# Kernel optimization log

Hardware: AMD Instinct MI355X
Metric: run time of the kernel (lower is better)

## Reference

```python
import jax, jax.numpy as jnp
import numpy as np

H = 2048          # hidden_size
NH = 32           # num_attention_heads
NKV = 8           # num_key_value_heads
HD = H // NH      # head_dim = 64
ROT = int(HD * 0.25)  # rotary_ndims = 16
THETA = 10000.0


def _rope_cos_sin(seq_len, position_ids):
    # inv_freq over the rotary dims
    inv_freq = 1.0 / (THETA ** (jnp.arange(0, ROT, 2, dtype=jnp.float32) / ROT))
    t = jnp.arange(seq_len, dtype=jnp.float32)
    freqs = jnp.outer(t, inv_freq)              # [S, ROT/2]
    emb = jnp.concatenate([freqs, freqs], -1)   # [S, ROT]
    cos = jnp.cos(emb)[position_ids][:, None]   # [B, 1, Q, ROT]
    sin = jnp.sin(emb)[position_ids][:, None]
    return cos, sin


def _rotate_half(x):
    x1, x2 = jnp.split(x, 2, axis=-1)
    return jnp.concatenate([-x2, x1], axis=-1)


def setup_inputs() -> dict:
    key = jax.random.key(0)
    ks = jax.random.split(key, 5)
    B, S = 2, 2048
    hidden_states = jax.random.normal(ks[0], (B, S, H), jnp.float32)
    # additive causal mask
    neg = jnp.finfo(jnp.float32).min
    causal = jnp.where(jnp.tril(jnp.ones((S, S), bool)), 0.0, neg).astype(jnp.float32)
    attention_mask = jnp.broadcast_to(causal[None, None], (B, 1, S, S))
    position_ids = jnp.broadcast_to(jnp.arange(S, dtype=jnp.int32)[None], (B, S))
    sc = 0.02
    Wq = jax.random.normal(ks[1], (H, H), jnp.float32) * sc
    Wk = jax.random.normal(ks[2], (NKV * HD, H), jnp.float32) * sc
    Wv = jax.random.normal(ks[3], (NKV * HD, H), jnp.float32) * sc
    Wo = jax.random.normal(ks[4], (H, H), jnp.float32) * sc
    return {"hidden_states": hidden_states, "attention_mask": attention_mask,
            "position_ids": position_ids, "Wq": Wq, "Wk": Wk, "Wv": Wv, "Wo": Wo}


def reference(hidden_states, attention_mask, position_ids, Wq, Wk, Wv, Wo):
    B, S, _ = hidden_states.shape
    q = (hidden_states @ Wq.T).reshape(B, S, NH, HD).transpose(0, 2, 1, 3)    # [B,NH,S,HD]
    k = (hidden_states @ Wk.T).reshape(B, S, NKV, HD).transpose(0, 2, 1, 3)   # [B,NKV,S,HD]
    v = (hidden_states @ Wv.T).reshape(B, S, NKV, HD).transpose(0, 2, 1, 3)

    cos, sin = _rope_cos_sin(S, position_ids)  # [B,1,S,ROT]
    q_rot, q_pass = q[..., :ROT], q[..., ROT:]
    k_rot, k_pass = k[..., :ROT], k[..., ROT:]
    q_rot = q_rot * cos + _rotate_half(q_rot) * sin
    k_rot = k_rot * cos + _rotate_half(k_rot) * sin
    q = jnp.concatenate([q_rot, q_pass], -1)
    k = jnp.concatenate([k_rot, k_pass], -1)

    # GQA without materializing repeated K/V: group Q heads per KV head
    G = NH // NKV
    qg = q.reshape(B, NKV, G, S, HD)
    scores = jnp.einsum('bhgqd,bhkd->bhgqk', qg, k) / np.sqrt(HD)
    scores = scores.reshape(B, NH, S, S) + attention_mask
    probs = jax.nn.softmax(scores.astype(jnp.float32), axis=-1).astype(q.dtype)
    out = jnp.einsum('bhgqk,bhkd->bhgqd', probs.reshape(B, NKV, G, S, S), v)
    out = out.reshape(B, NH, S, HD).transpose(0, 2, 1, 3).reshape(B, S, H)
    return out @ Wo.T
```

## Files before the change

kernel.cpp:

```cpp
#include <hip/hip_runtime.h>

typedef unsigned short u16;
typedef short s16x8 __attribute__((ext_vector_type(8)));
typedef u16 u16x8 __attribute__((ext_vector_type(8)));
typedef float f32x4 __attribute__((ext_vector_type(4)));
typedef __bf16 bf16x8 __attribute__((ext_vector_type(8)));

#define B_ 2
#define S_ 2048
#define H_ 2048
#define NH_ 32
#define NKV_ 8
#define HD_ 64
#define LDQ_ 3072
#define NTOK (B_ * S_)

__device__ __forceinline__ u16 f2bf(float f) {
  unsigned u = __float_as_uint(f);
  u += 0x7fffu + ((u >> 16) & 1u);
  return (u16)(u >> 16);
}
__device__ __forceinline__ float bf2f(u16 h) {
  return __uint_as_float(((unsigned)h) << 16);
}

__device__ __forceinline__ void gload16(const void* g, void* l) {
  __builtin_amdgcn_global_load_lds(
      (const __attribute__((address_space(1))) unsigned int*)g,
      (__attribute__((address_space(3))) unsigned int*)l, 16, 0, 0);
}

__device__ __forceinline__ f32x4 mfma16(s16x8 a, s16x8 b, f32x4 c) {
  return __builtin_amdgcn_mfma_f32_16x16x32_bf16(
      __builtin_bit_cast(bf16x8, a), __builtin_bit_cast(bf16x8, b), c, 0, 0, 0);
}

__global__ __launch_bounds__(256) void cvt_bf16(const float* __restrict__ src,
                                                u16* __restrict__ dst, int n8) {
  int i = blockIdx.x * 256 + threadIdx.x;
  if (i >= n8) return;
  const float4* s = (const float4*)src + (size_t)i * 2;
  float4 a = s[0], b = s[1];
  u16x8 o;
  o[0] = f2bf(a.x); o[1] = f2bf(a.y); o[2] = f2bf(a.z); o[3] = f2bf(a.w);
  o[4] = f2bf(b.x); o[5] = f2bf(b.y); o[6] = f2bf(b.z); o[7] = f2bf(b.w);
  *((u16x8*)dst + i) = o;
}

__global__ __launch_bounds__(256) void rope_table(float* __restrict__ tab) {
  int i = blockIdx.x * 256 + threadIdx.x;
  if (i >= S_ * 8) return;
  int p = i >> 3, k = i & 7;
  float inv = powf(10000.0f, -(float)k * 0.125f);
  float ang = (float)p * inv;
  tab[p * 16 + k] = cosf(ang);
  tab[p * 16 + 8 + k] = sinf(ang);
}

__global__ __launch_bounds__(256) void rope_apply(u16* __restrict__ C,
                                                  const int* __restrict__ pos,
                                                  const float* __restrict__ tab) {
  int t = blockIdx.x * 256 + threadIdx.x;
  if (t >= NTOK * 40) return;
  int token = t / 40, hh = t - token * 40;
  u16* p = C + (size_t)token * LDQ_ + (hh < 32 ? hh * 64 : 2048 + (hh - 32) * 64);
  const float* ct = tab + (size_t)pos[token] * 16;
  float x[16];
#pragma unroll
  for (int i = 0; i < 16; ++i) x[i] = bf2f(p[i]);
#pragma unroll
  for (int i = 0; i < 8; ++i) {
    float c = ct[i], s = ct[8 + i];
    p[i]     = f2bf(x[i] * c - x[i + 8] * s);
    p[i + 8] = f2bf(x[i + 8] * c + x[i] * s);
  }
}

__global__ __launch_bounds__(256) void vtrans(const u16* __restrict__ C,
                                              u16* __restrict__ Vt) {
  __shared__ u16 tile[64][72];
  int st = blockIdx.x;
  int kv = blockIdx.y;
  int tid = threadIdx.x;
  const u16* src = C + ((size_t)(kv >> 3) * S_ + (size_t)st * 64) * LDQ_ + 2560 + (kv & 7) * 64;
#pragma unroll
  for (int it = 0; it < 2; ++it) {
    int c = it * 256 + tid;
    int s = c >> 3, d0 = (c & 7) * 8;
    *(u16x8*)&tile[s][d0] = *(const u16x8*)(src + (size_t)s * LDQ_ + d0);
  }
  __syncthreads();
  u16* dst = Vt + (size_t)kv * HD_ * S_ + st * 64;
  int s = tid & 63;
#pragma unroll
  for (int it = 0; it < 16; ++it) {
    int d = it * 4 + (tid >> 6);
    dst[(size_t)d * S_ + s] = tile[s][d];
  }
}

__device__ __forceinline__ void store_c(u16* p, float v) { *p = f2bf(v); }
__device__ __forceinline__ void store_c(float* p, float v) { *p = v; }

template <typename OutT>
__global__ __launch_bounds__(256, 3) void gemm_bt(const u16* __restrict__ A,
                                                  const u16* __restrict__ Bw,
                                                  OutT* __restrict__ C,
                                                  int M, int N, int K) {
  __shared__ u16 lds[2 * 128 * 64];
  u16* ldsA = lds;
  u16* ldsB = lds + 128 * 64;
  const int tid = threadIdx.x;
  const int lane = tid & 63;
  const int wave = tid >> 6;
  const int wm = (wave & 1) * 64;
  const int wn = (wave >> 1) * 64;
  const int m0 = blockIdx.y * 128;
  const int n0 = blockIdx.x * 128;
  const int l15 = lane & 15;
  const int quad = lane >> 4;

  f32x4 acc[4][4];
#pragma unroll
  for (int i = 0; i < 4; ++i)
#pragma unroll
    for (int j = 0; j < 4; ++j) acc[i][j] = {0.f, 0.f, 0.f, 0.f};

  const u16* Ab = A + (size_t)m0 * K;
  const u16* Bb = Bw + (size_t)n0 * K;

  for (int k0 = 0; k0 < K; k0 += 64) {
    __syncthreads();
#pragma unroll
    for (int it = 0; it < 4; ++it) {
      int c = it * 256 + tid;
      int row = c >> 3;
      int kk = (c & 7) * 8;
      gload16(Ab + (size_t)row * K + k0 + kk, ldsA + (size_t)c * 8);
      gload16(Bb + (size_t)row * K + k0 + kk, ldsB + (size_t)c * 8);
    }
    __syncthreads();
#pragma unroll
    for (int ks = 0; ks < 2; ++ks) {
      int ko = ks * 32 + quad * 8;
      s16x8 af[4], bfr[4];
#pragma unroll
      for (int i = 0; i < 4; ++i)
        af[i] = *(const s16x8*)(ldsA + (size_t)(wm + i * 16 + l15) * 64 + ko);
#pragma unroll
      for (int j = 0; j < 4; ++j)
        bfr[j] = *(const s16x8*)(ldsB + (size_t)(wn + j * 16 + l15) * 64 + ko);
#pragma unroll
      for (int i = 0; i < 4; ++i)
#pragma unroll
        for (int j = 0; j < 4; ++j)
          acc[i][j] = mfma16(af[i], bfr[j], acc[i][j]);
    }
  }
#pragma unroll
  for (int i = 0; i < 4; ++i) {
    int row = m0 + wm + i * 16 + quad * 4;
#pragma unroll
    for (int j = 0; j < 4; ++j) {
      int col = n0 + wn + j * 16 + l15;
#pragma unroll
      for (int r = 0; r < 4; ++r) store_c(C + (size_t)(row + r) * N + col, acc[i][j][r]);
    }
  }
}

#define KSTRIDE 72
#define PSTRIDE 72
__global__ __launch_bounds__(256, 3) void flash_attn(const u16* __restrict__ QKV,
                                                     const u16* __restrict__ Vt,
                                                     u16* __restrict__ O) {
  __shared__ u16 Kl2[2][64 * KSTRIDE];
  __shared__ u16 Vl2[2][64 * KSTRIDE];
  __shared__ u16 Pb[4][16 * PSTRIDE];
  const int h = blockIdx.x;
  const int b = blockIdx.y;
  const int qt = 15 - (int)blockIdx.z;
  const int kvh = h >> 2;
  const int tid = threadIdx.x;
  const int lane = tid & 63;
  const int wave = tid >> 6;
  const int l15 = lane & 15;
  const int quad = lane >> 4;

  const u16* Qb = QKV + (size_t)b * S_ * LDQ_ + h * 64;
  const u16* Kb = QKV + (size_t)b * S_ * LDQ_ + 2048 + kvh * 64;
  const u16* Vb = Vt + (size_t)(b * 8 + kvh) * HD_ * S_;

  s16x8 qf[2][2];
#pragma unroll
  for (int g = 0; g < 2; ++g) {
    int qrow = qt * 128 + wave * 32 + g * 16 + l15;
#pragma unroll
    for (int ks = 0; ks < 2; ++ks)
      qf[g][ks] = *(const s16x8*)(Qb + (size_t)qrow * LDQ_ + ks * 32 + quad * 8);
  }

  f32x4 acc_o[2][4];
#pragma unroll
  for (int g = 0; g < 2; ++g)
#pragma unroll
    for (int nt = 0; nt < 4; ++nt) acc_o[g][nt] = {0.f, 0.f, 0.f, 0.f};
  float l_lane[2][4];
#pragma unroll
  for (int g = 0; g < 2; ++g)
#pragma unroll
    for (int r = 0; r < 4; ++r) l_lane[g][r] = 0.0f;

  const int r0 = tid >> 3, ch0 = (tid & 7) * 8;
  const int r1 = (tid + 256) >> 3, ch1 = (tid & 7) * 8;

  const int nkt = 2 * qt + 2;
  const int wrowmax = qt * 128 + wave * 32 + 31;
  const float SC = 0.18033688011112042f;
  const float M0 = 4.0f;

  u16x8 kr0, kr1, vr0, vr1;
  kr0 = *(const u16x8*)(Kb + (size_t)r0 * LDQ_ + ch0);
  kr1 = *(const u16x8*)(Kb + (size_t)r1 * LDQ_ + ch1);
  vr0 = *(const u16x8*)(Vb + (size_t)r0 * S_ + ch0);
  vr1 = *(const u16x8*)(Vb + (size_t)r1 * S_ + ch1);

  for (int kt = 0; kt < nkt; ++kt) {
    u16* Kl = Kl2[kt & 1];
    u16* Vl = Vl2[kt & 1];
    *(u16x8*)(Kl + r0 * KSTRIDE + ch0) = kr0;
    *(u16x8*)(Kl + r1 * KSTRIDE + ch1) = kr1;
    *(u16x8*)(Vl + r0 * KSTRIDE + ch0) = vr0;
    *(u16x8*)(Vl + r1 * KSTRIDE + ch1) = vr1;
    __syncthreads();
    if (kt + 1 < nkt) {
      int kb = (kt + 1) * 64;
      kr0 = *(const u16x8*)(Kb + (size_t)(kb + r0) * LDQ_ + ch0);
      kr1 = *(const u16x8*)(Kb + (size_t)(kb + r1) * LDQ_ + ch1);
      vr0 = *(const u16x8*)(Vb + (size_t)r0 * S_ + kb + ch0);
      vr1 = *(const u16x8*)(Vb + (size_t)r1 * S_ + kb + ch1);
    }
    if (kt * 64 <= wrowmax) {
      f32x4 sc[2][4];
#pragma unroll
      for (int nt = 0; nt < 4; ++nt) {
        const u16* kp = Kl + (nt * 16 + l15) * KSTRIDE + quad * 8;
        s16x8 k0 = *(const s16x8*)(kp);
        s16x8 k1 = *(const s16x8*)(kp + 32);
        f32x4 z = {0.f, 0.f, 0.f, 0.f};
        sc[0][nt] = mfma16(qf[0][1], k1, mfma16(qf[0][0], k0, z));
        sc[1][nt] = mfma16(qf[1][1], k1, mfma16(qf[1][0], k0, z));
      }
      u16* Pw = Pb[wave];
      s16x8 pf[2][2];
#pragma unroll
      for (int g = 0; g < 2; ++g) {
        const int row0 = qt * 128 + wave * 32 + g * 16;
        const bool diag = (kt * 64 + 63) > row0;
#pragma unroll
        for (int nt = 0; nt < 4; ++nt) {
          int scol = kt * 64 + nt * 16 + l15;
#pragma unroll
          for (int r = 0; r < 4; ++r) {
            float v = fmaf(sc[g][nt][r], SC, -M0);
            if (diag && scol > (row0 + quad * 4 + r)) v = -1e30f;
            float p = exp2f(v);
            sc[g][nt][r] = p;
            l_lane[g][r] += p;
          }
        }
#pragma unroll
        for (int nt = 0; nt < 4; ++nt)
#pragma unroll
          for (int r = 0; r < 4; ++r)
            Pw[(quad * 4 + r) * PSTRIDE + nt * 16 + l15] = f2bf(sc[g][nt][r]);
        const u16* pp = Pw + (size_t)l15 * PSTRIDE + quad * 8;
        pf[g][0] = *(const s16x8*)(pp);
        pf[g][1] = *(const s16x8*)(pp + 32);
      }
#pragma unroll
      for (int nt = 0; nt < 4; ++nt) {
        const u16* vp = Vl + (nt * 16 + l15) * KSTRIDE + quad * 8;
        s16x8 v0 = *(const s16x8*)(vp);
        s16x8 v1 = *(const s16x8*)(vp + 32);
        acc_o[0][nt] = mfma16(pf[0][1], v1, mfma16(pf[0][0], v0, acc_o[0][nt]));
        acc_o[1][nt] = mfma16(pf[1][1], v1, mfma16(pf[1][0], v0, acc_o[1][nt]));
      }
    }
  }
#pragma unroll
  for (int g = 0; g < 2; ++g)
#pragma unroll
    for (int r = 0; r < 4; ++r) {
      float l = l_lane[g][r];
#pragma unroll
      for (int off = 8; off; off >>= 1) l += __shfl_xor(l, off);
      float inv = 1.0f / l;
      int row = qt * 128 + wave * 32 + g * 16 + quad * 4 + r;
      size_t obase = ((size_t)b * S_ + row) * (size_t)H_ + h * 64;
#pragma unroll
      for (int nt = 0; nt < 4; ++nt)
        O[obase + nt * 16 + l15] = f2bf(acc_o[g][nt][r] * inv);
    }
}

extern "C" void kernel_launch(void* const* d_in, const int* in_sizes, int n_in,
                              void* d_out, int out_size, void* d_ws, size_t ws_size,
                              hipStream_t stream) {
  const float* hs = (const float*)d_in[0];
  const int* pos = (const int*)d_in[2];
  const float* Wq = (const float*)d_in[3];
  const float* Wk = (const float*)d_in[4];
  const float* Wv = (const float*)d_in[5];
  const float* Wo = (const float*)d_in[6];
  float* out = (float*)d_out;

  if (ws_size < 67239936) return;

  char* ws = (char*)d_ws;
  u16* Xbf   = (u16*)(ws);
  u16* Wqkv  = (u16*)(ws + 16777216);
  u16* Wob   = (u16*)(ws + 29360128);
  u16* Cqkv  = (u16*)(ws + 37748736);
  u16* Vt    = (u16*)(ws + 62914560);
  float* tab = (float*)(ws + 67108864);
  u16* O     = Xbf;

  cvt_bf16<<<4096, 256, 0, stream>>>(hs, Xbf, 1048576);
  cvt_bf16<<<2048, 256, 0, stream>>>(Wq, Wqkv, 524288);
  cvt_bf16<<<512, 256, 0, stream>>>(Wk, Wqkv + 4194304, 131072);
  cvt_bf16<<<512, 256, 0, stream>>>(Wv, Wqkv + 5242880, 131072);
  cvt_bf16<<<2048, 256, 0, stream>>>(Wo, Wob, 524288);
  rope_table<<<64, 256, 0, stream>>>(tab);

  gemm_bt<u16><<<dim3(24, 32), 256, 0, stream>>>(Xbf, Wqkv, Cqkv, 4096, 3072, 2048);
  rope_apply<<<640, 256, 0, stream>>>(Cqkv, pos, tab);
  vtrans<<<dim3(32, 16), 256, 0, stream>>>(Cqkv, Vt);
  flash_attn<<<dim3(32, 2, 16), 256, 0, stream>>>(Cqkv, Vt, O);
  gemm_bt<float><<<dim3(16, 32), 256, 0, stream>>>(O, Wob, out, 4096, 2048, 2048);
}
```

Measured before the change: 344.1 us.

## Fuse conversion launches and transpose score MFMA for cheaper softmax packing

Merges the five fp32-to-bf16 conversion kernels into one launch that picks the source by index range. In flash attention the score MFMA operands are swapped, so each lane holds a column of S^T. This lets the probabilities be packed with perm into 32-bit stores, uses the native exp2 builtin, applies a select-based causal mask only on diagonal tiles, and keeps the row sum as a per-lane vector reduced once at the end. It is meant to cut launch overhead and softmax ALU and LDS work, but it changes the P layout and uses round-half-up bf16 rounding instead of round-to-nearest-even.

```diff
diff --git a/kernel.cpp b/kernel.cpp
--- a/kernel.cpp
+++ b/kernel.cpp
@@ -35,16 +35,23 @@
       __builtin_bit_cast(bf16x8, a), __builtin_bit_cast(bf16x8, b), c, 0, 0, 0);
 }
 
-__global__ __launch_bounds__(256) void cvt_bf16(const float* __restrict__ src,
-                                                u16* __restrict__ dst, int n8) {
+__global__ __launch_bounds__(256) void cvt_all(const float* __restrict__ hs,
+    const float* __restrict__ wq, const float* __restrict__ wk,
+    const float* __restrict__ wv, const float* __restrict__ wo,
+    u16* __restrict__ xbf, u16* __restrict__ wqkv, u16* __restrict__ wob) {
   int i = blockIdx.x * 256 + threadIdx.x;
-  if (i >= n8) return;
-  const float4* s = (const float4*)src + (size_t)i * 2;
-  float4 a = s[0], b = s[1];
+  const float* s; u16* d; int j;
+  if (i < 1048576)      { s = hs; d = xbf;            j = i; }
+  else if (i < 1572864) { s = wq; d = wqkv;           j = i - 1048576; }
+  else if (i < 1703936) { s = wk; d = wqkv + 4194304; j = i - 1572864; }
+  else if (i < 1835008) { s = wv; d = wqkv + 5242880; j = i - 1703936; }
+  else                  { s = wo; d = wob;            j = i - 1835008; }
+  const float4* sp = (const float4*)s + (size_t)j * 2;
+  float4 a = sp[0], b = sp[1];
   u16x8 o;
   o[0] = f2bf(a.x); o[1] = f2bf(a.y); o[2] = f2bf(a.z); o[3] = f2bf(a.w);
   o[4] = f2bf(b.x); o[5] = f2bf(b.y); o[6] = f2bf(b.z); o[7] = f2bf(b.w);
-  *((u16x8*)dst + i) = o;
+  *((u16x8*)d + j) = o;
 }
 
 __global__ __launch_bounds__(256) void rope_table(float* __restrict__ tab) {
@@ -171,6 +178,34 @@
 
 #define KSTRIDE 72
 #define PSTRIDE 72
+#define SC_ 0.18033688011112042f
+#define M0_ 4.0f
+
+template <bool DIAG>
+__device__ __forceinline__ void softmax_pack(const f32x4* sc, f32x4& lacc,
+                                             u16* pwq, int sb, int qg) {
+#pragma unroll
+  for (int nt = 0; nt < 4; ++nt) {
+    f32x4 p;
+#pragma unroll
+    for (int r = 0; r < 4; ++r) {
+      float v = fmaf(sc[nt][r], SC_, -M0_);
+      float e = __builtin_amdgcn_exp2f(v);
+      if (DIAG) e = (sb + nt * 16 + r > qg) ? 0.0f : e;
+      p[r] = e;
+    }
+    lacc += p;
+    unsigned lo = __builtin_amdgcn_perm(__float_as_uint(p[1]) + 0x8000u,
+                                        __float_as_uint(p[0]) + 0x8000u,
+                                        0x07060302u);
+    unsigned hi = __builtin_amdgcn_perm(__float_as_uint(p[3]) + 0x8000u,
+                                        __float_as_uint(p[2]) + 0x8000u,
+                                        0x07060302u);
+    *(unsigned*)(pwq + nt * 16) = lo;
+    *(unsigned*)(pwq + nt * 16 + 2) = hi;
+  }
+}
+
 __global__ __launch_bounds__(256, 3) void flash_attn(const u16* __restrict__ QKV,
                                                      const u16* __restrict__ Vt,
                                                      u16* __restrict__ O) {
@@ -191,10 +226,12 @@
   const u16* Kb = QKV + (size_t)b * S_ * LDQ_ + 2048 + kvh * 64;
   const u16* Vb = Vt + (size_t)(b * 8 + kvh) * HD_ * S_;
 
+  const int row0w = qt * 128 + wave * 32;
+
   s16x8 qf[2][2];
 #pragma unroll
   for (int g = 0; g < 2; ++g) {
-    int qrow = qt * 128 + wave * 32 + g * 16 + l15;
+    int qrow = row0w + g * 16 + l15;
 #pragma unroll
     for (int ks = 0; ks < 2; ++ks)
       qf[g][ks] = *(const s16x8*)(Qb + (size_t)qrow * LDQ_ + ks * 32 + quad * 8);
@@ -205,19 +242,15 @@
   for (int g = 0; g < 2; ++g)
 #pragma unroll
     for (int nt = 0; nt < 4; ++nt) acc_o[g][nt] = {0.f, 0.f, 0.f, 0.f};
-  float l_lane[2][4];
-#pragma unroll
-  for (int g = 0; g < 2; ++g)
-#pragma unroll
-    for (int r = 0; r < 4; ++r) l_lane[g][r] = 0.0f;
+  f32x4 lacc[2] = {{0.f, 0.f, 0.f, 0.f}, {0.f, 0.f, 0.f, 0.f}};
 
   const int r0 = tid >> 3, ch0 = (tid & 7) * 8;
-  const int r1 = (tid + 256) >> 3, ch1 = (tid & 7) * 8;
+  const int r1 = r0 + 32, ch1 = ch0;
 
   const int nkt = 2 * qt + 2;
-  const int wrowmax = qt * 128 + wave * 32 + 31;
-  const float SC = 0.18033688011112042f;
-  const float M0 = 4.0f;
+
+  u16* Pwq = Pb[wave] + l15 * PSTRIDE + quad * 4;
+  const u16* Pr = Pb[wave] + l15 * PSTRIDE + quad * 8;
 
   u16x8 kr0, kr1, vr0, vr1;
   kr0 = *(const u16x8*)(Kb + (size_t)r0 * LDQ_ + ch0);
@@ -240,7 +273,7 @@
       vr0 = *(const u16x8*)(Vb + (size_t)r0 * S_ + kb + ch0);
       vr1 = *(const u16x8*)(Vb + (size_t)r1 * S_ + kb + ch1);
     }
-    if (kt * 64 <= wrowmax) {
+    if (kt * 64 <= row0w + 31) {
       f32x4 sc[2][4];
 #pragma unroll
       for (int nt = 0; nt < 4; ++nt) {
@@ -248,35 +281,20 @@
         s16x8 k0 = *(const s16x8*)(kp);
         s16x8 k1 = *(const s16x8*)(kp + 32);
         f32x4 z = {0.f, 0.f, 0.f, 0.f};
-        sc[0][nt] = mfma16(qf[0][1], k1, mfma16(qf[0][0], k0, z));
-        sc[1][nt] = mfma16(qf[1][1], k1, mfma16(qf[1][0], k0, z));
+        sc[0][nt] = mfma16(k1, qf[0][1], mfma16(k0, qf[0][0], z));
+        sc[1][nt] = mfma16(k1, qf[1][1], mfma16(k0, qf[1][0], z));
       }
-      u16* Pw = Pb[wave];
+      const int sb = kt * 64 + quad * 4;
       s16x8 pf[2][2];
 #pragma unroll
       for (int g = 0; g < 2; ++g) {
-        const int row0 = qt * 128 + wave * 32 + g * 16;
-        const bool diag = (kt * 64 + 63) > row0;
-#pragma unroll
-        for (int nt = 0; nt < 4; ++nt) {
-          int scol = kt * 64 + nt * 16 + l15;
-#pragma unroll
-          for (int r = 0; r < 4; ++r) {
-            float v = fmaf(sc[g][nt][r], SC, -M0);
-            if (diag && scol > (row0 + quad * 4 + r)) v = -1e30f;
-            float p = exp2f(v);
-            sc[g][nt][r] = p;
-            l_lane[g][r] += p;
-          }
-        }
-#pragma unroll
-        for (int nt = 0; nt < 4; ++nt)
-#pragma unroll
-          for (int r = 0; r < 4; ++r)
-            Pw[(quad * 4 + r) * PSTRIDE + nt * 16 + l15] = f2bf(sc[g][nt][r]);
-        const u16* pp = Pw + (size_t)l15 * PSTRIDE + quad * 8;
-        pf[g][0] = *(const s16x8*)(pp);
-        pf[g][1] = *(const s16x8*)(pp + 32);
+        const int row0 = row0w + g * 16;
+        if (kt * 64 + 63 > row0)
+          softmax_pack<true>(sc[g], lacc[g], Pwq, sb, row0 + l15);
+        else
+          softmax_pack<false>(sc[g], lacc[g], Pwq, sb, row0 + l15);
+        pf[g][0] = *(const s16x8*)(Pr);
+        pf[g][1] = *(const s16x8*)(Pr + 32);
       }
 #pragma unroll
       for (int nt = 0; nt < 4; ++nt) {
@@ -289,19 +307,21 @@
     }
   }
 #pragma unroll
-  for (int g = 0; g < 2; ++g)
+  for (int g = 0; g < 2; ++g) {
+    float l = (lacc[g][0] + lacc[g][1]) + (lacc[g][2] + lacc[g][3]);
+    l += __shfl_xor(l, 16);
+    l += __shfl_xor(l, 32);
 #pragma unroll
     for (int r = 0; r < 4; ++r) {
-      float l = l_lane[g][r];
-#pragma unroll
-      for (int off = 8; off; off >>= 1) l += __shfl_xor(l, off);
-      float inv = 1.0f / l;
-      int row = qt * 128 + wave * 32 + g * 16 + quad * 4 + r;
+      float ls = __shfl(l, quad * 4 + r);
+      float inv = 1.0f / ls;
+      int row = row0w + g * 16 + quad * 4 + r;
       size_t obase = ((size_t)b * S_ + row) * (size_t)H_ + h * 64;
 #pragma unroll
       for (int nt = 0; nt < 4; ++nt)
         O[obase + nt * 16 + l15] = f2bf(acc_o[g][nt][r] * inv);
     }
+  }
 }
 
 extern "C" void kernel_launch(void* const* d_in, const int* in_sizes, int n_in,
@@ -326,11 +346,7 @@
   float* tab = (float*)(ws + 67108864);
   u16* O     = Xbf;
 
-  cvt_bf16<<<4096, 256, 0, stream>>>(hs, Xbf, 1048576);
-  cvt_bf16<<<2048, 256, 0, stream>>>(Wq, Wqkv, 524288);
-  cvt_bf16<<<512, 256, 0, stream>>>(Wk, Wqkv + 4194304, 131072);
-  cvt_bf16<<<512, 256, 0, stream>>>(Wv, Wqkv + 5242880, 131072);
-  cvt_bf16<<<2048, 256, 0, stream>>>(Wo, Wob, 524288);
+  cvt_all<<<9216, 256, 0, stream>>>(hs, Wq, Wk, Wv, Wo, Xbf, Wqkv, Wob);
   rope_table<<<64, 256, 0, stream>>>(tab);
 
   gemm_bt<u16><<<dim3(24, 32), 256, 0, stream>>>(Xbf, Wqkv, Cqkv, 4096, 3072, 2048);
```

Measured after the change: 312.1 us. 9.3% less time.
